# Optimization experiments

Hardware: AMD Instinct MI355X
Metric: run time of the kernel (lower is better)

Reference implementation:

```python
import jax, jax.numpy as jnp
import numpy as np
import math

D_MODEL = 1024
D_STATE = 64
DT_MIN, DT_MAX = 1e-3, 1e-1


def setup_inputs() -> dict:
    key = jax.random.key(0)
    ks = jax.random.split(key, 8)
    x = jax.random.normal(ks[0], (2, 4096, D_MODEL), dtype=jnp.float32)
    # in_proj / out_proj: nn.Linear default init (kaiming-uniform-ish); uniform is fine for a reference
    lim = 1.0 / math.sqrt(D_MODEL)
    Win = jax.random.uniform(ks[1], (D_MODEL, D_MODEL), minval=-lim, maxval=lim, dtype=jnp.float32)
    bin_ = jax.random.uniform(ks[2], (D_MODEL,), minval=-lim, maxval=lim, dtype=jnp.float32)
    Wout = jax.random.uniform(ks[3], (D_MODEL, D_MODEL), minval=-lim, maxval=lim, dtype=jnp.float32)
    bout = jax.random.uniform(ks[4], (D_MODEL,), minval=-lim, maxval=lim, dtype=jnp.float32)
    # HiPPO-LegS style init: A_log[d, n] = log(n + 1)
    A_log = jnp.broadcast_to(jnp.log(jnp.arange(1, D_STATE + 1, dtype=jnp.float32)), (D_MODEL, D_STATE))
    B = 0.1 * jax.random.normal(ks[5], (D_MODEL, D_STATE), dtype=jnp.float32)
    C = 0.1 * jax.random.normal(ks[6], (D_MODEL, D_STATE), dtype=jnp.float32)
    Dp = jnp.ones((D_MODEL,), dtype=jnp.float32)
    log_dt = jax.random.uniform(ks[7], (D_MODEL,), dtype=jnp.float32) * (math.log(DT_MAX) - math.log(DT_MIN)) + math.log(DT_MIN)
    dt = jnp.exp(log_dt)
    return {"x": x, "Win": Win, "bin_": bin_, "A_log": A_log, "B": B, "C": C,
            "Dp": Dp, "dt": dt, "Wout": Wout, "bout": bout}


def reference(x, Win, bin_, A_log, B, C, Dp, dt, Wout, bout):
    b, L, d = x.shape
    x = x @ Win.T + bin_                      # in_proj
    u = jnp.transpose(x, (0, 2, 1))           # [b, d, l]
    A = -jnp.exp(-A_log)                      # [d, n], negative real poles
    logdA = A * dt[:, None]                   # log(dA) since dA = exp(A*dt) > 0
    dB = B * dt[:, None]                      # [d, n]
    t = jnp.arange(L, dtype=x.dtype)
    # dA**t == exp(t * log dA): vectorized Vandermonde, replaces per-step power loop
    powers = jnp.exp(logdA[:, :, None] * t)   # [d, n, L]
    k = jnp.einsum('dn,dnl->dl', C * dB, powers)  # SSM conv kernel [d, L]
    n_fft = 2 * L
    k_f = jnp.fft.rfft(k, n=n_fft)            # [d, F]
    u_f = jnp.fft.rfft(u, n=n_fft)            # [b, d, F]
    y = jnp.fft.irfft(u_f * k_f[None], n=n_fft)[..., :L]  # causal conv
    y = y + u * Dp[:, None]                   # skip connection
    y = jnp.transpose(y, (0, 2, 1))           # [b, l, d]
    return y @ Wout.T + bout                  # out_proj
```

## Files before the change

kernel.cpp:

```cpp
#include <hip/hip_runtime.h>
#include <cstdint>
#include <cstddef>

#define D_MODEL 1024
#define D_STATE 64
#define SEQ     4096
#define BATCH   2
#define MROWS   (BATCH*SEQ)

typedef __bf16 bf16x8 __attribute__((ext_vector_type(8)));
typedef float  f32x4  __attribute__((ext_vector_type(4)));
typedef unsigned short u16;
typedef unsigned int   u32;

union BF8 { bf16x8 v; uint4 q; u16 e[8]; };

__device__ __forceinline__ u16 f2bf(float x) {
    u32 u = __float_as_uint(x);
    u32 r = u + 0x7FFFu + ((u >> 16) & 1u);
    return (u16)(r >> 16);
}
__device__ __forceinline__ float bf2f(u16 h) {
    return __uint_as_float(((u32)h) << 16);
}
__device__ __forceinline__ uint4 pack8u(const u16* e) {
    return make_uint4((u32)e[0] | ((u32)e[1] << 16), (u32)e[2] | ((u32)e[3] << 16),
                      (u32)e[4] | ((u32)e[5] << 16), (u32)e[6] | ((u32)e[7] << 16));
}

__device__ __forceinline__ void async16(const void* g, void* l) {
    __builtin_amdgcn_global_load_lds(
        (const __attribute__((address_space(1))) unsigned int*)(uintptr_t)g,
        (__attribute__((address_space(3))) unsigned int*)(uintptr_t)l,
        16, 0, 0);
}

__global__ __launch_bounds__(256) void prep_kernel(
    const float* __restrict__ x, const float* __restrict__ Win,
    const float* __restrict__ Wout,
    u16* __restrict__ Ax, u16* __restrict__ Bw1, u16* __restrict__ Bw2)
{
    const size_t base = (size_t)blockIdx.x * 4096 + threadIdx.x * 4;
    const float* src; u16* dst; size_t off;
    if (base < 8388608)        { src = x;    dst = Ax;  off = base; }
    else if (base < 9437184)   { src = Win;  dst = Bw1; off = base - 8388608; }
    else                       { src = Wout; dst = Bw2; off = base - 9437184; }
    #pragma unroll
    for (int i = 0; i < 4; ++i) {
        const float4 v = *reinterpret_cast<const float4*>(src + off + i * 1024);
        *reinterpret_cast<uint2*>(dst + off + i * 1024) =
            make_uint2((u32)f2bf(v.x) | ((u32)f2bf(v.y) << 16),
                       (u32)f2bf(v.z) | ((u32)f2bf(v.w) << 16));
    }
}

template<int MODE>
__global__ __launch_bounds__(256) void gemm_bt(
    const u16* __restrict__ A, const u16* __restrict__ Bm,
    const float* __restrict__ bias, float* __restrict__ out)
{
    __shared__ __align__(16) u16 As[2][128 * 64];
    __shared__ __align__(16) u16 Bs[2][128 * 64];
    const int bid  = blockIdx.x;
    const int slot = bid >> 3;
    const int m0 = ((bid & 7) * 8 + (slot >> 3)) * 128;
    const int n0 = (slot & 7) * 128;
    const int tid = threadIdx.x;
    const int wave = tid >> 6, lane = tid & 63;
    const int wm = wave >> 1, wn = wave & 1;
    const int qm = lane & 15, qk = lane >> 4;
    f32x4 acc[4][4] = {};

    auto stage = [&](u16* Ad, u16* Bd, int k0) {
        #pragma unroll
        for (int it = 0; it < 4; ++it) {
            const int c   = it * 256 + tid;
            const int row = c >> 3, col = (c & 7) * 8;
            const int ldsbase = (it * 256 + wave * 64) * 8;
            async16(&A[(size_t)(m0 + row) * D_MODEL + k0 + col], Ad + ldsbase);
            async16(&Bm[(size_t)(n0 + row) * D_MODEL + k0 + col], Bd + ldsbase);
        }
    };
    auto compute = [&](const u16* As_, const u16* Bs_) {
        #pragma unroll
        for (int kk = 0; kk < 2; ++kk) {
            bf16x8 af[4], bg[4];
            #pragma unroll
            for (int i = 0; i < 4; ++i) {
                af[i] = *reinterpret_cast<const bf16x8*>(&As_[(wm*64 + i*16 + qm)*64 + kk*32 + qk*8]);
                bg[i] = *reinterpret_cast<const bf16x8*>(&Bs_[(wn*64 + i*16 + qm)*64 + kk*32 + qk*8]);
            }
            #pragma unroll
            for (int i = 0; i < 4; ++i)
                #pragma unroll
                for (int j = 0; j < 4; ++j)
                    acc[i][j] = __builtin_amdgcn_mfma_f32_16x16x32_bf16(af[i], bg[j], acc[i][j], 0, 0, 0);
        }
    };

    stage(As[0], Bs[0], 0);
    __syncthreads();
    #pragma unroll 1
    for (int kp = 0; kp < 7; ++kp) {
        stage(As[1], Bs[1], 128 * kp + 64);
        compute(As[0], Bs[0]);
        __syncthreads();
        stage(As[0], Bs[0], 128 * kp + 128);
        compute(As[1], Bs[1]);
        __syncthreads();
    }
    stage(As[1], Bs[1], 960);
    compute(As[0], Bs[0]);
    __syncthreads();
    compute(As[1], Bs[1]);

    if (MODE == 0) {
        #pragma unroll
        for (int i = 0; i < 4; ++i) {
            const int r0 = m0 + wm*64 + i*16 + qk*4;
            #pragma unroll
            for (int j = 0; j < 4; ++j) {
                const int c = n0 + wn*64 + j*16 + qm;
                const float bv = bias[c];
                #pragma unroll
                for (int reg = 0; reg < 4; ++reg)
                    out[(size_t)(r0 + reg) * D_MODEL + c] = acc[i][j][reg] + bv;
            }
        }
    } else {
        float* Tt = reinterpret_cast<float*>(&As[0][0]);
        float* T = &Tt[wave * 16 * 65];
        float bvj[4];
        #pragma unroll
        for (int j = 0; j < 4; ++j) bvj[j] = bias[n0 + wn*64 + j*16 + qm];
        const int dcol = n0 + wn*64 + lane;
        #pragma unroll
        for (int i = 0; i < 4; ++i) {
            #pragma unroll
            for (int j = 0; j < 4; ++j)
                #pragma unroll
                for (int reg = 0; reg < 4; ++reg)
                    T[(qk*4 + reg) * 65 + j*16 + qm] = acc[i][j][reg] + bvj[j];
            __builtin_amdgcn_wave_barrier();
            float4 o[4];
            #pragma unroll
            for (int t4 = 0; t4 < 4; ++t4)
                o[t4] = make_float4(T[(t4*4 + 0) * 65 + lane], T[(t4*4 + 1) * 65 + lane],
                                    T[(t4*4 + 2) * 65 + lane], T[(t4*4 + 3) * 65 + lane]);
            const int r0 = m0 + wm*64 + i*16;
            const int bb = r0 >> 12, l0 = r0 & (SEQ - 1);
            float* dst = &out[((size_t)(bb * D_MODEL + dcol)) * SEQ + l0];
            #pragma unroll
            for (int t4 = 0; t4 < 4; ++t4)
                reinterpret_cast<float4*>(dst)[t4] = o[t4];
            __builtin_amdgcn_wave_barrier();
        }
    }
}

__global__ __launch_bounds__(128) void scan2_kernel(
    float* __restrict__ ut, const float* __restrict__ A_log,
    const float* __restrict__ Bp, const float* __restrict__ Cp,
    const float* __restrict__ dtp, const float* __restrict__ Dpv)
{
    __shared__ __align__(16) u16 KT_s[64 * 64];
    __shared__ __align__(16) u16 RA_s[64 * 64];
    __shared__ __align__(16) u16 P2_s[64 * 64];
    __shared__ __align__(16) u16 SH[2][64 * 64];
    const int d = blockIdx.x, tid = threadIdx.x;
    const int w = tid >> 6, lane = tid & 63;
    const int qm = lane & 15, qk = lane >> 4;

    const float dt_d  = dtp[d];
    const float logdA = -expf(-A_log[d * D_STATE + lane]) * dt_d;
    const float r     = expf(logdA);
    const float dBn   = Bp[d * D_STATE + lane] * dt_d;
    const float Cv    = Cp[d * D_STATE + lane];
    const float rTn   = expf(logdA * 64.0f);
    const float Dpd   = Dpv[d];

    float* ug = ut + ((size_t)(w * D_MODEL + d)) * SEQ;

    float* dB_sh = reinterpret_cast<float*>(&SH[0][0]);
    float* w_sh  = dB_sh + 64;
    float* k_sh  = dB_sh + 128;

    bf16x8 Uf[4][4];
    #pragma unroll
    for (int ct = 0; ct < 4; ++ct) {
        const float* src = ug + (ct * 16 + qm) * 64;
        #pragma unroll
        for (int jb = 0; jb < 2; ++jb) {
            const float4 v0 = *reinterpret_cast<const float4*>(src + jb * 32 + qk * 8);
            const float4 v1 = *reinterpret_cast<const float4*>(src + jb * 32 + qk * 8 + 4);
            const float fv[8] = {v0.x, v0.y, v0.z, v0.w, v1.x, v1.y, v1.z, v1.w};
            BF8 hi, lo;
            #pragma unroll
            for (int i = 0; i < 8; ++i) {
                hi.e[i] = f2bf(fv[i]);
                lo.e[i] = f2bf(fv[i] - bf2f(hi.e[i]));
            }
            Uf[ct][jb]     = hi.v;
            Uf[ct][jb + 2] = lo.v;
        }
    }

    if (w == 0) {
        dB_sh[lane] = dBn;
        w_sh[lane]  = Cv * dBn;
        for (int o = 0; o < 8; ++o) {
            float tmp[8];
            tmp[7] = expf(logdA * (float)(63 - (o * 8 + 7)));
            #pragma unroll
            for (int i = 6; i >= 0; --i) tmp[i] = tmp[i + 1] * r;
            u16 e[8];
            #pragma unroll
            for (int i = 0; i < 8; ++i) e[i] = f2bf(tmp[i]);
            *reinterpret_cast<uint4*>(&RA_s[lane * 64 + o * 8]) = pack8u(e);
        }
    } else {
        float p = Cv;
        for (int t = 0; t < 64; ++t) { p *= r; P2_s[t * 64 + lane] = f2bf(p); }
    }
    __syncthreads();
    if (w == 0) {
        float kacc = 0.f;
        if (lane == 0) {
            for (int n = 0; n < 64; ++n) kacc += w_sh[n];
        } else {
            const u16* prow = &P2_s[(lane - 1) * 64];
            for (int o = 0; o < 8; ++o) {
                BF8 p8; p8.q = *reinterpret_cast<const uint4*>(&prow[o * 8]);
                #pragma unroll
                for (int i = 0; i < 8; ++i) kacc += dB_sh[o * 8 + i] * bf2f(p8.e[i]);
            }
        }
        k_sh[lane] = kacc;
        for (int o = 0; o < 8; ++o) {
            u16 e[8];
            #pragma unroll
            for (int i = 0; i < 8; ++i) {
                const int j = o * 8 + i;
                e[i] = (j <= lane) ? f2bf(k_sh[lane - j]) : (u16)0;
            }
            *reinterpret_cast<uint4*>(&KT_s[lane * 64 + o * 8]) = pack8u(e);
        }
    }
    __syncthreads();

    u16* sh = SH[w];
    {
        bf16x8 Af[4][2];
        #pragma unroll
        for (int nt = 0; nt < 4; ++nt)
            #pragma unroll
            for (int jb = 0; jb < 2; ++jb)
                Af[nt][jb] = *reinterpret_cast<const bf16x8*>(
                    &RA_s[(nt * 16 + qm) * 64 + jb * 32 + qk * 8]);
        f32x4 acc[4][4] = {};
        #pragma unroll
        for (int kk = 0; kk < 4; ++kk)
            #pragma unroll
            for (int nt = 0; nt < 4; ++nt)
                #pragma unroll
                for (int ct = 0; ct < 4; ++ct)
                    acc[nt][ct] = __builtin_amdgcn_mfma_f32_16x16x32_bf16(
                        Af[nt][kk & 1], Uf[ct][kk], acc[nt][ct], 0, 0, 0);
        #pragma unroll
        for (int nt = 0; nt < 4; ++nt)
            #pragma unroll
            for (int ct = 0; ct < 4; ++ct) {
                const int c = ct * 16 + qm, nn0 = nt * 16 + qk * 4;
                uint2 pk;
                pk.x = (u32)f2bf(acc[nt][ct][0]) | ((u32)f2bf(acc[nt][ct][1]) << 16);
                pk.y = (u32)f2bf(acc[nt][ct][2]) | ((u32)f2bf(acc[nt][ct][3]) << 16);
                *reinterpret_cast<uint2*>(&sh[c * 64 + nn0]) = pk;
            }
    }
    __syncthreads();

    {
        float h = 0.f;
        u16* col = sh + lane;
        for (int b = 0; b < 4; ++b) {
            float sb[16];
            #pragma unroll
            for (int i = 0; i < 16; ++i) sb[i] = bf2f(col[(b * 16 + i) * 64]);
            #pragma unroll
            for (int i = 0; i < 16; ++i) {
                col[(b * 16 + i) * 64] = f2bf(h);
                h = rTn * h + dBn * sb[i];
            }
        }
    }
    __syncthreads();

    {
        bf16x8 Af[4][2];
        #pragma unroll
        for (int tt = 0; tt < 4; ++tt)
            #pragma unroll
            for (int jb = 0; jb < 2; ++jb)
                Af[tt][jb] = *reinterpret_cast<const bf16x8*>(
                    &KT_s[(tt * 16 + qm) * 64 + jb * 32 + qk * 8]);
        f32x4 acc[4][4] = {};
        #pragma unroll
        for (int kk = 0; kk < 4; ++kk)
            #pragma unroll
            for (int tt = 0; tt < 4; ++tt)
                #pragma unroll
                for (int ct = 0; ct < 4; ++ct)
                    acc[tt][ct] = __builtin_amdgcn_mfma_f32_16x16x32_bf16(
                        Af[tt][kk & 1], Uf[ct][kk], acc[tt][ct], 0, 0, 0);
        bf16x8 Pf[4][2];
        #pragma unroll
        for (int tt = 0; tt < 4; ++tt)
            #pragma unroll
            for (int kb = 0; kb < 2; ++kb)
                Pf[tt][kb] = *reinterpret_cast<const bf16x8*>(
                    &P2_s[(tt * 16 + qm) * 64 + kb * 32 + qk * 8]);
        #pragma unroll
        for (int ct = 0; ct < 4; ++ct)
            #pragma unroll
            for (int kb = 0; kb < 2; ++kb) {
                const bf16x8 Hf = *reinterpret_cast<const bf16x8*>(
                    &sh[(ct * 16 + qm) * 64 + kb * 32 + qk * 8]);
                #pragma unroll
                for (int tt = 0; tt < 4; ++tt)
                    acc[tt][ct] = __builtin_amdgcn_mfma_f32_16x16x32_bf16(
                        Pf[tt][kb], Hf, acc[tt][ct], 0, 0, 0);
            }
        #pragma unroll
        for (int tt = 0; tt < 4; ++tt)
            #pragma unroll
            for (int ct = 0; ct < 4; ++ct) {
                const int c = ct * 16 + qm, t0 = tt * 16 + qk * 4;
                float* dst = ug + c * 64 + t0;
                const float4 u4 = *reinterpret_cast<const float4*>(dst);
                float4 y;
                y.x = acc[tt][ct][0] + Dpd * u4.x;
                y.y = acc[tt][ct][1] + Dpd * u4.y;
                y.z = acc[tt][ct][2] + Dpd * u4.z;
                y.w = acc[tt][ct][3] + Dpd * u4.w;
                *reinterpret_cast<float4*>(dst) = y;
            }
    }
}

__global__ __launch_bounds__(256) void trans_kernel(
    const float* __restrict__ yt, u16* __restrict__ Ax)
{
    __shared__ float T[64 * 68];
    const int b = blockIdx.z, dx = blockIdx.y * 64, lx = blockIdx.x * 64;
    const int tid = threadIdx.x;
    const int t16 = tid >> 4, l16 = tid & 15;
    #pragma unroll
    for (int ii = 0; ii < 4; ++ii) {
        const int dd = ii * 16 + t16;
        const int ll = l16 * 4;
        float4 v = *reinterpret_cast<const float4*>(
            &yt[((size_t)(b * D_MODEL + dx + dd)) * SEQ + lx + ll]);
        *reinterpret_cast<float4*>(&T[dd * 68 + ll]) = v;
    }
    __syncthreads();
    #pragma unroll
    for (int ii = 0; ii < 4; ++ii) {
        const int ll = ii * 16 + t16;
        const int dd = l16 * 4;
        float v0 = T[(dd + 0) * 68 + ll], v1 = T[(dd + 1) * 68 + ll];
        float v2 = T[(dd + 2) * 68 + ll], v3 = T[(dd + 3) * 68 + ll];
        const size_t row = (size_t)b * SEQ + lx + ll;
        *reinterpret_cast<uint2*>(Ax + row * D_MODEL + dx + dd) =
            make_uint2((u32)f2bf(v0) | ((u32)f2bf(v1) << 16),
                       (u32)f2bf(v2) | ((u32)f2bf(v3) << 16));
    }
}

extern "C" void kernel_launch(void* const* d_in, const int* in_sizes, int n_in,
                              void* d_out, int out_size, void* d_ws, size_t ws_size,
                              hipStream_t stream) {
    const float* x     = (const float*)d_in[0];
    const float* Win   = (const float*)d_in[1];
    const float* bin   = (const float*)d_in[2];
    const float* A_log = (const float*)d_in[3];
    const float* Bp    = (const float*)d_in[4];
    const float* Cp    = (const float*)d_in[5];
    const float* Dpv   = (const float*)d_in[6];
    const float* dtp   = (const float*)d_in[7];
    const float* Wout  = (const float*)d_in[8];
    const float* bout  = (const float*)d_in[9];
    float* out = (float*)d_out;

    char* ws = (char*)d_ws;
    u16*   Ax  = (u16*)(ws);
    float* ut  = (float*)(ws + (size_t)25165824);
    u16*   Bw1 = (u16*)(ws + (size_t)58720256);
    u16*   Bw2 = (u16*)(ws + (size_t)60817408);

    prep_kernel<<<2560, 256, 0, stream>>>(x, Win, Wout, Ax, Bw1, Bw2);
    gemm_bt<1><<<512, 256, 0, stream>>>(Ax, Bw1, bin, ut);
    scan2_kernel<<<D_MODEL, 128, 0, stream>>>(ut, A_log, Bp, Cp, dtp, Dpv);
    trans_kernel<<<dim3(SEQ / 64, D_MODEL / 64, BATCH), 256, 0, stream>>>(ut, Ax);
    gemm_bt<0><<<512, 256, 0, stream>>>(Ax, Bw2, bout, out);
}
```

Baseline: 188.3 us.

## Restructure bf16 GEMM into 128x256 tiles with triple-buffered swizzled LDS pipeline

The GEMM kernel now uses 512-thread blocks, each computing a 128x256 output tile. Shared memory holds a three-stage ring buffer whose addresses are XOR-swizzled to avoid bank conflicts. Each k-step is split into four compute phases, and the async global-to-LDS loads for two steps ahead are spread across those phases, with s_setprio and fine-grained vmcnt waits. The aim is to hide global load latency, improve MFMA utilization and cut LDS bank conflicts. The cost is more LDS per block, more barriers, and an epilogue that depends on the new wave layout being consistent.

```diff
diff --git a/kernel.cpp b/kernel.cpp
--- a/kernel.cpp
+++ b/kernel.cpp
@@ -54,65 +54,96 @@
     }
 }
 
+#define PHASE(QI, QJ, STG)                                                    \
+    {                                                                         \
+        bf16x8 af[2][2], bg[2][2];                                            \
+        _Pragma("unroll") for (int f = 0; f < 2; ++f) {                       \
+            const int ar = wm * 64 + QI * 32 + f * 16 + qm;                   \
+            const int br = wn * 64 + QJ * 32 + f * 16 + qm;                   \
+            _Pragma("unroll") for (int kk = 0; kk < 2; ++kk) {                \
+                const int ca = kk * 4 + qk;                                   \
+                af[f][kk] = *reinterpret_cast<const bf16x8*>(                 \
+                    &Ab[ar * 64 + ((ca ^ (ar & 7)) << 3)]);                   \
+                bg[f][kk] = *reinterpret_cast<const bf16x8*>(                 \
+                    &Bb[br * 64 + ((ca ^ (br & 7)) << 3)]);                   \
+            }                                                                 \
+        }                                                                     \
+        STG;                                                                  \
+        __builtin_amdgcn_s_barrier();                                         \
+        asm volatile("s_waitcnt lgkmcnt(0)" ::: "memory");                    \
+        __builtin_amdgcn_s_setprio(1);                                        \
+        _Pragma("unroll") for (int kk = 0; kk < 2; ++kk)                      \
+        _Pragma("unroll") for (int f = 0; f < 2; ++f)                         \
+        _Pragma("unroll") for (int g = 0; g < 2; ++g)                         \
+            acc[QI*2+f][QJ*2+g] = __builtin_amdgcn_mfma_f32_16x16x32_bf16(    \
+                af[f][kk], bg[g][kk], acc[QI*2+f][QJ*2+g], 0, 0, 0);          \
+        __builtin_amdgcn_s_setprio(0);                                        \
+    }
+
 template<int MODE>
-__global__ __launch_bounds__(256) void gemm_bt(
+__global__ __launch_bounds__(512, 2) void gemm_bt(
     const u16* __restrict__ A, const u16* __restrict__ Bm,
     const float* __restrict__ bias, float* __restrict__ out)
 {
-    __shared__ __align__(16) u16 As[2][128 * 64];
-    __shared__ __align__(16) u16 Bs[2][128 * 64];
-    const int bid  = blockIdx.x;
-    const int slot = bid >> 3;
-    const int m0 = ((bid & 7) * 8 + (slot >> 3)) * 128;
-    const int n0 = (slot & 7) * 128;
-    const int tid = threadIdx.x;
+    __shared__ __align__(16) u16 L[73728];
+    const int bid = blockIdx.x;
+    const int id  = (bid & 7) * 32 + (bid >> 3);
+    const int m0  = (id >> 2) * 128;
+    const int n0  = (id & 3) * 256;
+    const int tid  = threadIdx.x;
     const int wave = tid >> 6, lane = tid & 63;
-    const int wm = wave >> 1, wn = wave & 1;
+    const int wm = wave >> 2, wn = wave & 3;
     const int qm = lane & 15, qk = lane >> 4;
     f32x4 acc[4][4] = {};
 
-    auto stage = [&](u16* Ad, u16* Bd, int k0) {
-        #pragma unroll
-        for (int it = 0; it < 4; ++it) {
-            const int c   = it * 256 + tid;
-            const int row = c >> 3, col = (c & 7) * 8;
-            const int ldsbase = (it * 256 + wave * 64) * 8;
-            async16(&A[(size_t)(m0 + row) * D_MODEL + k0 + col], Ad + ldsbase);
-            async16(&Bm[(size_t)(n0 + row) * D_MODEL + k0 + col], Bd + ldsbase);
-        }
+    u16* const Abuf = L;
+    u16* const Bbuf = L + 24576;
+
+    auto stageA = [&](int b, int k0, int it) {
+        const int chunk = it * 512 + wave * 64 + lane;
+        const int row = chunk >> 3, c16 = chunk & 7;
+        async16(&A[(size_t)(m0 + row) * D_MODEL + k0 + ((c16 ^ (row & 7)) << 3)],
+                Abuf + b * 8192 + (it * 512 + wave * 64) * 8);
     };
-    auto compute = [&](const u16* As_, const u16* Bs_) {
-        #pragma unroll
-        for (int kk = 0; kk < 2; ++kk) {
-            bf16x8 af[4], bg[4];
-            #pragma unroll
-            for (int i = 0; i < 4; ++i) {
-                af[i] = *reinterpret_cast<const bf16x8*>(&As_[(wm*64 + i*16 + qm)*64 + kk*32 + qk*8]);
-                bg[i] = *reinterpret_cast<const bf16x8*>(&Bs_[(wn*64 + i*16 + qm)*64 + kk*32 + qk*8]);
-            }
-            #pragma unroll
-            for (int i = 0; i < 4; ++i)
-                #pragma unroll
-                for (int j = 0; j < 4; ++j)
-                    acc[i][j] = __builtin_amdgcn_mfma_f32_16x16x32_bf16(af[i], bg[j], acc[i][j], 0, 0, 0);
-        }
+    auto stageB = [&](int b, int k0, int it) {
+        const int chunk = it * 512 + wave * 64 + lane;
+        const int row = chunk >> 3, c16 = chunk & 7;
+        async16(&Bm[(size_t)(n0 + row) * D_MODEL + k0 + ((c16 ^ (row & 7)) << 3)],
+                Bbuf + b * 16384 + (it * 512 + wave * 64) * 8);
     };
 
-    stage(As[0], Bs[0], 0);
-    __syncthreads();
+    #pragma unroll
+    for (int it = 0; it < 2; ++it) stageA(0, 0, it);
+    #pragma unroll
+    for (int it = 0; it < 4; ++it) stageB(0, 0, it);
+    #pragma unroll
+    for (int it = 0; it < 2; ++it) stageA(1, 64, it);
+    #pragma unroll
+    for (int it = 0; it < 4; ++it) stageB(1, 64, it);
+    asm volatile("s_waitcnt vmcnt(6)" ::: "memory");
+    __builtin_amdgcn_s_barrier();
+
+    int cur = 0;
     #pragma unroll 1
-    for (int kp = 0; kp < 7; ++kp) {
-        stage(As[1], Bs[1], 128 * kp + 64);
-        compute(As[0], Bs[0]);
-        __syncthreads();
-        stage(As[0], Bs[0], 128 * kp + 128);
-        compute(As[1], Bs[1]);
-        __syncthreads();
-    }
-    stage(As[1], Bs[1], 960);
-    compute(As[0], Bs[0]);
-    __syncthreads();
-    compute(As[1], Bs[1]);
+    for (int t = 0; t < 16; ++t) {
+        const u16* Ab = Abuf + cur * 8192;
+        const u16* Bb = Bbuf + cur * 16384;
+        const int nxt = (cur == 0) ? 2 : cur - 1;
+        const int ks  = (t + 2) * 64;
+        const bool st = t < 14;
+        PHASE(0, 0, if (st) { stageA(nxt, ks, 0); stageA(nxt, ks, 1); })
+        __builtin_amdgcn_s_barrier();
+        PHASE(0, 1, if (st) { stageB(nxt, ks, 0); stageB(nxt, ks, 1); })
+        __builtin_amdgcn_s_barrier();
+        PHASE(1, 0, if (st) { stageB(nxt, ks, 2); stageB(nxt, ks, 3); })
+        __builtin_amdgcn_s_barrier();
+        PHASE(1, 1, ;)
+        if (t < 14)       asm volatile("s_waitcnt vmcnt(6)" ::: "memory");
+        else if (t == 14) asm volatile("s_waitcnt vmcnt(0)" ::: "memory");
+        __builtin_amdgcn_s_barrier();
+        cur = (cur == 2) ? 0 : cur + 1;
+    }
+    __syncthreads();
 
     if (MODE == 0) {
         #pragma unroll
@@ -128,7 +159,7 @@
             }
         }
     } else {
-        float* Tt = reinterpret_cast<float*>(&As[0][0]);
+        float* Tt = reinterpret_cast<float*>(&L[0]);
         float* T = &Tt[wave * 16 * 65];
         float bvj[4];
         #pragma unroll
@@ -398,8 +429,8 @@
     u16*   Bw2 = (u16*)(ws + (size_t)60817408);
 
     prep_kernel<<<2560, 256, 0, stream>>>(x, Win, Wout, Ax, Bw1, Bw2);
-    gemm_bt<1><<<512, 256, 0, stream>>>(Ax, Bw1, bin, ut);
+    gemm_bt<1><<<256, 512, 0, stream>>>(Ax, Bw1, bin, ut);
     scan2_kernel<<<D_MODEL, 128, 0, stream>>>(ut, A_log, Bp, Cp, dtp, Dpv);
     trans_kernel<<<dim3(SEQ / 64, D_MODEL / 64, BATCH), 256, 0, stream>>>(ut, Ax);
-    gemm_bt<0><<<512, 256, 0, stream>>>(Ax, Bw2, bout, out);
-}
+    gemm_bt<0><<<256, 512, 0, stream>>>(Ax, Bw2, bout, out);
+}
```

Measured after the change: 191.2 us. Within noise of the previous version (+1.5%).
